# Kernel optimization log

Measured on AMD Instinct MI355X. Metric: run time of the kernel, lower is better.

Reference implementation:

```python
import jax, jax.numpy as jnp
import numpy as np

H = 16
D_MODEL = 1024
B, S = 2, 2048
DH = D_MODEL // H


def setup_inputs() -> dict:
    key = jax.random.key(0)
    ks = jax.random.split(key, 12)
    std = 0.02
    q = jax.random.normal(ks[0], (B, S, D_MODEL), dtype=jnp.float32)
    k = jax.random.normal(ks[1], (B, S, D_MODEL), dtype=jnp.float32)
    v = jax.random.normal(ks[2], (B, S, D_MODEL), dtype=jnp.float32)
    # additive causal mask: 0 on/below diagonal, -1e9 above
    causal = jnp.tril(jnp.ones((S, S), dtype=bool))
    mask = jnp.where(causal, 0.0, -1e9).astype(jnp.float32)[None, None, :, :]
    def dense(kk):
        return (jax.random.normal(kk, (D_MODEL, D_MODEL), dtype=jnp.float32) * std,
                jnp.zeros((D_MODEL,), dtype=jnp.float32))
    Wq, bq = dense(ks[3])
    Wk, bk = dense(ks[4])
    Wv, bv = dense(ks[5])
    Wo, bo = dense(ks[6])
    return {"q": q, "k": k, "v": v, "mask": mask,
            "Wq": Wq, "bq": bq, "Wk": Wk, "bk": bk,
            "Wv": Wv, "bv": bv, "Wo": Wo, "bo": bo}


def reference(q, k, v, mask, Wq, bq, Wk, bk, Wv, bv, Wo, bo):
    b, s, d = q.shape
    def split_heads(x):  # [b,s,d] -> [b,h,s,dh]
        return x.reshape(b, s, H, DH).transpose(0, 2, 1, 3)
    qh = split_heads(q @ Wq + bq)
    kh = split_heads(k @ Wk + bk)
    vh = split_heads(v @ Wv + bv)
    scale = 1.0 / jnp.sqrt(jnp.asarray(DH, dtype=qh.dtype))
    scores = jnp.einsum('bhqd,bhkd->bhqk', qh, kh) * scale + mask
    weights = jax.nn.softmax(scores, axis=-1)
    ctx = jnp.einsum('bhqk,bhkd->bhqd', weights, vh)
    ctx = ctx.transpose(0, 2, 1, 3).reshape(b, s, d)
    return ctx @ Wo + bo
```

## Files before the change

kernel.cpp:

```cpp
#include <hip/hip_runtime.h>
#include <hip/hip_bf16.h>
#include <stdint.h>

typedef __bf16 bf16x8 __attribute__((ext_vector_type(8)));
typedef float  f32x4  __attribute__((ext_vector_type(4)));
typedef __hip_bfloat16 bf16_t;

#define D_MODEL 1024
#define NH 16
#define DH 64
#define BB 2
#define SS 2048
#define MTOT (BB*SS)
#define NQT (SS/64)

#define GBM 128
#define GBN 128
#define GBK 64

__global__ void cvt_qkv_kernel(const float* __restrict__ q, const float* __restrict__ k,
                               const float* __restrict__ v, bf16_t* __restrict__ dst) {
  const int n1v = MTOT * D_MODEL / 4;
  int tid = blockIdx.x * blockDim.x + threadIdx.x;
  int stride = gridDim.x * blockDim.x;
  for (int i = tid; i < 3 * n1v; i += stride) {
    int which = i / n1v;
    int j = i - which * n1v;
    const float4* src = (const float4*)(which == 0 ? q : (which == 1 ? k : v));
    float4 f = src[j];
    union { bf16_t h[4]; short4 s4; } u;
    u.h[0] = __float2bfloat16(f.x);
    u.h[1] = __float2bfloat16(f.y);
    u.h[2] = __float2bfloat16(f.z);
    u.h[3] = __float2bfloat16(f.w);
    ((short4*)dst)[(size_t)which * n1v + j] = u.s4;
  }
}

__global__ void transpose_w_kernel(const float* __restrict__ W0, const float* __restrict__ W1,
                                   const float* __restrict__ W2, const float* __restrict__ W3,
                                   bf16_t* __restrict__ WtAll) {
  __shared__ float tile[32][33];
  const int z = blockIdx.z;
  const float* W = (z == 0) ? W0 : (z == 1) ? W1 : (z == 2) ? W2 : W3;
  bf16_t* Wt = WtAll + (size_t)z * D_MODEL * D_MODEL;
  const int tx = threadIdx.x, ty = threadIdx.y;
  const int bx = blockIdx.x, by = blockIdx.y;
#pragma unroll
  for (int i = 0; i < 4; ++i)
    tile[ty + i * 8][tx] = W[(size_t)(by * 32 + ty + i * 8) * D_MODEL + bx * 32 + tx];
  __syncthreads();
#pragma unroll
  for (int i = 0; i < 4; ++i)
    Wt[(size_t)(bx * 32 + ty + i * 8) * D_MODEL + by * 32 + tx] =
        __float2bfloat16(tile[tx][ty + i * 8]);
}

__device__ __forceinline__ void g2lds16(const bf16_t* g, bf16_t* l) {
  __builtin_amdgcn_global_load_lds((__attribute__((address_space(1))) void*)(g),
                                   (__attribute__((address_space(3))) void*)(l), 16, 0, 0);
}

__device__ __forceinline__ void gemm_tile_mainloop(const bf16_t* __restrict__ A,
                                                   const bf16_t* __restrict__ Bt,
                                                   bf16_t* As, bf16_t* Bs,
                                                   int m0, int n0, f32x4 acc[4][4]) {
  const int tid = threadIdx.x;
  const int wv = tid >> 6, ln = tid & 63;
  const int wr = wv >> 1, wc = wv & 1;
  const int lr = ln & 15, lg = ln >> 4;

#pragma unroll
  for (int mi = 0; mi < 4; ++mi)
#pragma unroll
    for (int ni = 0; ni < 4; ++ni)
      acc[mi][ni] = (f32x4){0.f, 0.f, 0.f, 0.f};

  for (int kt = 0; kt < D_MODEL / GBK; ++kt) {
#pragma unroll
    for (int c = 0; c < 4; ++c) {
      int chunk = wv * 4 + c;
      int row = chunk * 8 + (ln >> 3);
      int col = (ln & 7) * 8;
      g2lds16(A  + (size_t)(m0 + row) * D_MODEL + kt * GBK + col, As + chunk * 8 * GBK);
      g2lds16(Bt + (size_t)(n0 + row) * D_MODEL + kt * GBK + col, Bs + chunk * 8 * GBK);
    }
    __syncthreads();
#pragma unroll
    for (int ks = 0; ks < 2; ++ks) {
      bf16x8 af[4], bfr[4];
#pragma unroll
      for (int mi = 0; mi < 4; ++mi)
        af[mi] = *(const bf16x8*)(As + (size_t)(wr * 64 + mi * 16 + lr) * GBK + ks * 32 + lg * 8);
#pragma unroll
      for (int ni = 0; ni < 4; ++ni)
        bfr[ni] = *(const bf16x8*)(Bs + (size_t)(wc * 64 + ni * 16 + lr) * GBK + ks * 32 + lg * 8);
#pragma unroll
      for (int mi = 0; mi < 4; ++mi)
#pragma unroll
        for (int ni = 0; ni < 4; ++ni)
          acc[mi][ni] = __builtin_amdgcn_mfma_f32_16x16x32_bf16(af[mi], bfr[ni], acc[mi][ni], 0, 0, 0);
    }
    __syncthreads();
  }
}

__global__ __launch_bounds__(256)
void proj_gemm_kernel(const bf16_t* __restrict__ Aq, const bf16_t* __restrict__ Ak,
                      const bf16_t* __restrict__ Av, const bf16_t* __restrict__ WtAll,
                      const float* __restrict__ bq, const float* __restrict__ bk,
                      const float* __restrict__ bv,
                      bf16_t* __restrict__ Qg, bf16_t* __restrict__ Kg,
                      bf16_t* __restrict__ Vt) {
  __shared__ bf16_t As[GBM * GBK];
  __shared__ bf16_t Bs[GBN * GBK];
  const int z = blockIdx.z;
  const bf16_t* A = (z == 0) ? Aq : (z == 1) ? Ak : Av;
  const bf16_t* Bt = WtAll + (size_t)z * D_MODEL * D_MODEL;
  const float* bias = (z == 0) ? bq : (z == 1) ? bk : bv;
  const int m0 = blockIdx.y * GBM, n0 = blockIdx.x * GBN;

  f32x4 acc[4][4];
  gemm_tile_mainloop(A, Bt, As, Bs, m0, n0, acc);

  const int tid = threadIdx.x;
  const int wv = tid >> 6, ln = tid & 63;
  const int wr = wv >> 1, wc = wv & 1;
  const int lr = ln & 15, lg = ln >> 4;

#pragma unroll
  for (int mi = 0; mi < 4; ++mi) {
#pragma unroll
    for (int ni = 0; ni < 4; ++ni) {
      int ncol = n0 + wc * 64 + ni * 16 + lr;
      float bsv = bias[ncol];
#pragma unroll
      for (int j = 0; j < 4; ++j) {
        int mrow = m0 + wr * 64 + mi * 16 + lg * 4 + j;
        bf16_t hv = __float2bfloat16(acc[mi][ni][j] + bsv);
        if (z == 0) {
          Qg[(size_t)mrow * D_MODEL + ncol] = hv;
        } else if (z == 1) {
          Kg[(size_t)mrow * D_MODEL + ncol] = hv;
        } else {
          int b = mrow >> 11, s = mrow & (SS - 1);
          Vt[(size_t)((b << 10) | ncol) * SS + s] = hv;
        }
      }
    }
  }
}

__global__ __launch_bounds__(256)
void out_gemm_kernel(const bf16_t* __restrict__ Ctx, const bf16_t* __restrict__ Wto,
                     const float* __restrict__ bo, float* __restrict__ out) {
  __shared__ bf16_t As[GBM * GBK];
  __shared__ bf16_t Bs[GBN * GBK];
  const int m0 = blockIdx.y * GBM, n0 = blockIdx.x * GBN;

  f32x4 acc[4][4];
  gemm_tile_mainloop(Ctx, Wto, As, Bs, m0, n0, acc);

  const int tid = threadIdx.x;
  const int wv = tid >> 6, ln = tid & 63;
  const int wr = wv >> 1, wc = wv & 1;
  const int lr = ln & 15, lg = ln >> 4;

#pragma unroll
  for (int mi = 0; mi < 4; ++mi) {
#pragma unroll
    for (int ni = 0; ni < 4; ++ni) {
      int ncol = n0 + wc * 64 + ni * 16 + lr;
      float bsv = bo[ncol];
#pragma unroll
      for (int j = 0; j < 4; ++j) {
        int mrow = m0 + wr * 64 + mi * 16 + lg * 4 + j;
        out[(size_t)mrow * D_MODEL + ncol] = acc[mi][ni][j] + bsv;
      }
    }
  }
}

__global__ __launch_bounds__(128)
void attn_kernel(const bf16_t* __restrict__ Qg, const bf16_t* __restrict__ Kg,
                 const bf16_t* __restrict__ Vt, bf16_t* __restrict__ Ctx) {
  __shared__ __align__(16) bf16_t P_lds[2][32][72];
  const int bh = blockIdx.x;
  const int pr = blockIdx.y;
  const int b = bh >> 4, h = bh & 15;
  const int wv = threadIdx.x >> 6, ln = threadIdx.x & 63;
  const int lr = ln & 15, lg = ln >> 4;

  const size_t qkbase = (size_t)b * SS * D_MODEL + (size_t)h * DH;
  const bf16_t* Kbase = Kg + qkbase;
  const bf16_t* Vbase = Vt + (size_t)(bh * 64) * SS;

  bf16x8 onesf;
#pragma unroll
  for (int j = 0; j < 8; ++j) onesf[j] = (__bf16)1.0f;

  for (int half = 0; half < 2; ++half) {
    const int qt = half ? (NQT - 1 - pr) : pr;
    const int q0 = qt * 64 + wv * 32;

    bf16x8 qf[2][2];
#pragma unroll
    for (int mi = 0; mi < 2; ++mi)
#pragma unroll
      for (int ks = 0; ks < 2; ++ks) {
        bf16x8 raw = *(const bf16x8*)(Qg + qkbase + (size_t)(q0 + mi * 16 + lr) * D_MODEL + ks * 32 + lg * 8);
#pragma unroll
        for (int j = 0; j < 8; ++j) raw[j] = (__bf16)((float)raw[j] * 0.125f);
        qf[mi][ks] = raw;
      }

    f32x4 acc_o[2][4];
    f32x4 acc_l[2];
    float m_run[2][4];
#pragma unroll
    for (int mi = 0; mi < 2; ++mi) {
#pragma unroll
      for (int db = 0; db < 4; ++db) acc_o[mi][db] = (f32x4){0.f, 0.f, 0.f, 0.f};
      acc_l[mi] = (f32x4){0.f, 0.f, 0.f, 0.f};
#pragma unroll
      for (int j = 0; j < 4; ++j) m_run[mi][j] = -1e30f;
    }

    bf16x8 kf_cur[2][4];
#pragma unroll
    for (int ks = 0; ks < 2; ++ks)
#pragma unroll
      for (int kb = 0; kb < 4; ++kb)
        kf_cur[ks][kb] = *(const bf16x8*)(Kbase + (size_t)(kb * 16 + lr) * D_MODEL + ks * 32 + lg * 8);

    const int ntiles = qt + 1;
    for (int t = 0; t < ntiles; ++t) {
      const int kv0 = t * 64;
      f32x4 sc[2][4];
#pragma unroll
      for (int mi = 0; mi < 2; ++mi)
#pragma unroll
        for (int kb = 0; kb < 4; ++kb) sc[mi][kb] = (f32x4){0.f, 0.f, 0.f, 0.f};

      __builtin_amdgcn_s_setprio(1);
#pragma unroll
      for (int ks = 0; ks < 2; ++ks) {
#pragma unroll
        for (int kb = 0; kb < 4; ++kb) {
          sc[0][kb] = __builtin_amdgcn_mfma_f32_16x16x32_bf16(qf[0][ks], kf_cur[ks][kb], sc[0][kb], 0, 0, 0);
          sc[1][kb] = __builtin_amdgcn_mfma_f32_16x16x32_bf16(qf[1][ks], kf_cur[ks][kb], sc[1][kb], 0, 0, 0);
        }
      }
      __builtin_amdgcn_s_setprio(0);

      bf16x8 kf_nxt[2][4];
      if (t + 1 < ntiles) {
#pragma unroll
        for (int ks = 0; ks < 2; ++ks)
#pragma unroll
          for (int kb = 0; kb < 4; ++kb)
            kf_nxt[ks][kb] = *(const bf16x8*)(Kbase + (size_t)(kv0 + 64 + kb * 16 + lr) * D_MODEL + ks * 32 + lg * 8);
      }
      bf16x8 vf[2][4];
#pragma unroll
      for (int ks = 0; ks < 2; ++ks)
#pragma unroll
        for (int db = 0; db < 4; ++db)
          vf[ks][db] = *(const bf16x8*)(Vbase + (size_t)(db * 16 + lr) * SS + kv0 + ks * 32 + lg * 8);

      if (kv0 + 63 > q0) {
#pragma unroll
        for (int mi = 0; mi < 2; ++mi)
#pragma unroll
          for (int kb = 0; kb < 4; ++kb)
#pragma unroll
            for (int j = 0; j < 4; ++j) {
              int kc = kv0 + kb * 16 + lr;
              int qr = q0 + mi * 16 + lg * 4 + j;
              if (kc > qr) sc[mi][kb][j] = -1e30f;
            }
      }

#pragma unroll
      for (int mi = 0; mi < 2; ++mi) {
#pragma unroll
        for (int j = 0; j < 4; ++j) {
          float vmax = fmaxf(fmaxf(sc[mi][0][j], sc[mi][1][j]), fmaxf(sc[mi][2][j], sc[mi][3][j]));
#pragma unroll
          for (int off = 1; off < 16; off <<= 1) vmax = fmaxf(vmax, __shfl_xor(vmax, off, 64));
          float mo = m_run[mi][j];
          float mn = fmaxf(mo, vmax);
          float scl = __expf(mo - mn);
          m_run[mi][j] = mn;
#pragma unroll
          for (int kb = 0; kb < 4; ++kb) {
            float p = __expf(sc[mi][kb][j] - mn);
            P_lds[wv][mi * 16 + lg * 4 + j][kb * 16 + lr] = __float2bfloat16(p);
          }
          acc_l[mi][j] *= scl;
#pragma unroll
          for (int db = 0; db < 4; ++db) acc_o[mi][db][j] *= scl;
        }
      }

      asm volatile("s_waitcnt lgkmcnt(0)" ::: "memory");
      __builtin_amdgcn_sched_barrier(0);

      __builtin_amdgcn_s_setprio(1);
#pragma unroll
      for (int ks = 0; ks < 2; ++ks) {
        bf16x8 pa0 = *(const bf16x8*)(&P_lds[wv][lr][ks * 32 + lg * 8]);
        bf16x8 pa1 = *(const bf16x8*)(&P_lds[wv][16 + lr][ks * 32 + lg * 8]);
        acc_l[0] = __builtin_amdgcn_mfma_f32_16x16x32_bf16(pa0, onesf, acc_l[0], 0, 0, 0);
        acc_l[1] = __builtin_amdgcn_mfma_f32_16x16x32_bf16(pa1, onesf, acc_l[1], 0, 0, 0);
#pragma unroll
        for (int db = 0; db < 4; ++db) {
          acc_o[0][db] = __builtin_amdgcn_mfma_f32_16x16x32_bf16(pa0, vf[ks][db], acc_o[0][db], 0, 0, 0);
          acc_o[1][db] = __builtin_amdgcn_mfma_f32_16x16x32_bf16(pa1, vf[ks][db], acc_o[1][db], 0, 0, 0);
        }
      }
      __builtin_amdgcn_s_setprio(0);

      if (t + 1 < ntiles) {
#pragma unroll
        for (int ks = 0; ks < 2; ++ks)
#pragma unroll
          for (int kb = 0; kb < 4; ++kb)
            kf_cur[ks][kb] = kf_nxt[ks][kb];
      }
    }

#pragma unroll
    for (int mi = 0; mi < 2; ++mi)
#pragma unroll
      for (int db = 0; db < 4; ++db)
#pragma unroll
        for (int j = 0; j < 4; ++j) {
          int qr = q0 + mi * 16 + lg * 4 + j;
          float val = acc_o[mi][db][j] / acc_l[mi][j];
          Ctx[(size_t)(b * SS + qr) * D_MODEL + h * DH + db * 16 + lr] = __float2bfloat16(val);
        }
  }
}

extern "C" void kernel_launch(void* const* d_in, const int* in_sizes, int n_in,
                              void* d_out, int out_size, void* d_ws, size_t ws_size,
                              hipStream_t stream) {
  const float* q  = (const float*)d_in[0];
  const float* k  = (const float*)d_in[1];
  const float* v  = (const float*)d_in[2];
  const float* bq = (const float*)d_in[5];
  const float* bk = (const float*)d_in[7];
  const float* bv = (const float*)d_in[9];
  const float* bo = (const float*)d_in[11];
  const float* Wq = (const float*)d_in[4];
  const float* Wk = (const float*)d_in[6];
  const float* Wv = (const float*)d_in[8];
  const float* Wo = (const float*)d_in[10];
  float* out = (float*)d_out;

  char* w = (char*)d_ws;
  bf16_t* Aqkv  = (bf16_t*)(w);
  bf16_t* WtAll = (bf16_t*)(w + 25165824);
  bf16_t* Qg    = (bf16_t*)(w + 33554432);
  bf16_t* Kg    = (bf16_t*)(w + 41943040);
  bf16_t* Vt    = (bf16_t*)(w + 50331648);
  bf16_t* Ctx   = (bf16_t*)(w + 58720256);

  cvt_qkv_kernel<<<2048, 256, 0, stream>>>(q, k, v, Aqkv);
  transpose_w_kernel<<<dim3(32, 32, 4), dim3(32, 8), 0, stream>>>(Wq, Wk, Wv, Wo, WtAll);
  proj_gemm_kernel<<<dim3(8, 32, 3), 256, 0, stream>>>(
      Aqkv, Aqkv + (size_t)MTOT * D_MODEL, Aqkv + 2 * (size_t)MTOT * D_MODEL,
      WtAll, bq, bk, bv, Qg, Kg, Vt);
  attn_kernel<<<dim3(32, 16), 128, 0, stream>>>(Qg, Kg, Vt, Ctx);
  out_gemm_kernel<<<dim3(8, 32), 256, 0, stream>>>(
      Ctx, WtAll + 3 * (size_t)D_MODEL * D_MODEL, bo, out);
}
```

Measured before the change: 299.1 us.

## Split attention KV range across four waves with split-K softmax merge

The attention block now runs four waves instead of two. Waves 0-1 process the low query tile and then the first part of the high tile's KV range. Waves 2-3 process the remaining KV tiles of the high query tile. Their partial O, max and sum are combined through shared memory with a log-sum-exp merge. The aim is to balance work and double the waves per block so the long causal rows finish sooner, at the cost of extra LDS, a block barrier and the merge arithmetic.

```diff
diff --git a/kernel.cpp b/kernel.cpp
--- a/kernel.cpp
+++ b/kernel.cpp
@@ -181,17 +181,156 @@
   }
 }
 
-__global__ __launch_bounds__(128)
+__device__ __forceinline__ void attn_run(
+    f32x4 acc_o[2][4], f32x4 acc_l[2], float m_run[2][4],
+    const bf16x8 qf[2][2], const bf16_t* Kbase, const bf16_t* Vbase,
+    bf16_t (*P)[72], int q0, int t0, int t1, int lr, int lg, bf16x8 onesf) {
+  bf16x8 kf_cur[2][4];
+#pragma unroll
+  for (int ks = 0; ks < 2; ++ks)
+#pragma unroll
+    for (int kb = 0; kb < 4; ++kb)
+      kf_cur[ks][kb] = *(const bf16x8*)(Kbase + (size_t)(t0 * 64 + kb * 16 + lr) * D_MODEL + ks * 32 + lg * 8);
+
+  for (int t = t0; t < t1; ++t) {
+    const int kv0 = t * 64;
+    f32x4 sc[2][4];
+#pragma unroll
+    for (int mi = 0; mi < 2; ++mi)
+#pragma unroll
+      for (int kb = 0; kb < 4; ++kb) sc[mi][kb] = (f32x4){0.f, 0.f, 0.f, 0.f};
+
+    __builtin_amdgcn_s_setprio(1);
+#pragma unroll
+    for (int ks = 0; ks < 2; ++ks) {
+#pragma unroll
+      for (int kb = 0; kb < 4; ++kb) {
+        sc[0][kb] = __builtin_amdgcn_mfma_f32_16x16x32_bf16(qf[0][ks], kf_cur[ks][kb], sc[0][kb], 0, 0, 0);
+        sc[1][kb] = __builtin_amdgcn_mfma_f32_16x16x32_bf16(qf[1][ks], kf_cur[ks][kb], sc[1][kb], 0, 0, 0);
+      }
+    }
+    __builtin_amdgcn_s_setprio(0);
+
+    bf16x8 kf_nxt[2][4];
+    if (t + 1 < t1) {
+#pragma unroll
+      for (int ks = 0; ks < 2; ++ks)
+#pragma unroll
+        for (int kb = 0; kb < 4; ++kb)
+          kf_nxt[ks][kb] = *(const bf16x8*)(Kbase + (size_t)(kv0 + 64 + kb * 16 + lr) * D_MODEL + ks * 32 + lg * 8);
+    }
+    bf16x8 vf[2][4];
+#pragma unroll
+    for (int ks = 0; ks < 2; ++ks)
+#pragma unroll
+      for (int db = 0; db < 4; ++db)
+        vf[ks][db] = *(const bf16x8*)(Vbase + (size_t)(db * 16 + lr) * SS + kv0 + ks * 32 + lg * 8);
+
+    if (kv0 + 63 > q0) {
+#pragma unroll
+      for (int mi = 0; mi < 2; ++mi)
+#pragma unroll
+        for (int kb = 0; kb < 4; ++kb)
+#pragma unroll
+          for (int j = 0; j < 4; ++j) {
+            int kc = kv0 + kb * 16 + lr;
+            int qr = q0 + mi * 16 + lg * 4 + j;
+            if (kc > qr) sc[mi][kb][j] = -1e30f;
+          }
+    }
+
+#pragma unroll
+    for (int mi = 0; mi < 2; ++mi) {
+#pragma unroll
+      for (int j = 0; j < 4; ++j) {
+        float vmax = fmaxf(fmaxf(sc[mi][0][j], sc[mi][1][j]), fmaxf(sc[mi][2][j], sc[mi][3][j]));
+#pragma unroll
+        for (int off = 1; off < 16; off <<= 1) vmax = fmaxf(vmax, __shfl_xor(vmax, off, 64));
+        float mo = m_run[mi][j];
+        float mn = fmaxf(mo, vmax);
+        float scl = __expf(mo - mn);
+        m_run[mi][j] = mn;
+#pragma unroll
+        for (int kb = 0; kb < 4; ++kb) {
+          float p = __expf(sc[mi][kb][j] - mn);
+          P[mi * 16 + lg * 4 + j][kb * 16 + lr] = __float2bfloat16(p);
+        }
+        acc_l[mi][j] *= scl;
+#pragma unroll
+        for (int db = 0; db < 4; ++db) acc_o[mi][db][j] *= scl;
+      }
+    }
+
+    asm volatile("s_waitcnt lgkmcnt(0)" ::: "memory");
+    __builtin_amdgcn_sched_barrier(0);
+
+    __builtin_amdgcn_s_setprio(1);
+#pragma unroll
+    for (int ks = 0; ks < 2; ++ks) {
+      bf16x8 pa0 = *(const bf16x8*)(&P[lr][ks * 32 + lg * 8]);
+      bf16x8 pa1 = *(const bf16x8*)(&P[16 + lr][ks * 32 + lg * 8]);
+      acc_l[0] = __builtin_amdgcn_mfma_f32_16x16x32_bf16(pa0, onesf, acc_l[0], 0, 0, 0);
+      acc_l[1] = __builtin_amdgcn_mfma_f32_16x16x32_bf16(pa1, onesf, acc_l[1], 0, 0, 0);
+#pragma unroll
+      for (int db = 0; db < 4; ++db) {
+        acc_o[0][db] = __builtin_amdgcn_mfma_f32_16x16x32_bf16(pa0, vf[ks][db], acc_o[0][db], 0, 0, 0);
+        acc_o[1][db] = __builtin_amdgcn_mfma_f32_16x16x32_bf16(pa1, vf[ks][db], acc_o[1][db], 0, 0, 0);
+      }
+    }
+    __builtin_amdgcn_s_setprio(0);
+
+    if (t + 1 < t1) {
+#pragma unroll
+      for (int ks = 0; ks < 2; ++ks)
+#pragma unroll
+        for (int kb = 0; kb < 4; ++kb)
+          kf_cur[ks][kb] = kf_nxt[ks][kb];
+    }
+  }
+}
+
+__device__ __forceinline__ void attn_load_q(bf16x8 qf[2][2], const bf16_t* Qbase,
+                                            int q0, int lr, int lg) {
+#pragma unroll
+  for (int mi = 0; mi < 2; ++mi)
+#pragma unroll
+    for (int ks = 0; ks < 2; ++ks) {
+      bf16x8 raw = *(const bf16x8*)(Qbase + (size_t)(q0 + mi * 16 + lr) * D_MODEL + ks * 32 + lg * 8);
+#pragma unroll
+      for (int j = 0; j < 8; ++j) raw[j] = (__bf16)((float)raw[j] * 0.125f);
+      qf[mi][ks] = raw;
+    }
+}
+
+__device__ __forceinline__ void attn_init(f32x4 acc_o[2][4], f32x4 acc_l[2], float m_run[2][4]) {
+#pragma unroll
+  for (int mi = 0; mi < 2; ++mi) {
+#pragma unroll
+    for (int db = 0; db < 4; ++db) acc_o[mi][db] = (f32x4){0.f, 0.f, 0.f, 0.f};
+    acc_l[mi] = (f32x4){0.f, 0.f, 0.f, 0.f};
+#pragma unroll
+    for (int j = 0; j < 4; ++j) m_run[mi][j] = -1e30f;
+  }
+}
+
+__global__ __launch_bounds__(256)
 void attn_kernel(const bf16_t* __restrict__ Qg, const bf16_t* __restrict__ Kg,
                  const bf16_t* __restrict__ Vt, bf16_t* __restrict__ Ctx) {
-  __shared__ __align__(16) bf16_t P_lds[2][32][72];
+  __shared__ __align__(16) bf16_t P_lds[4][32][72];
+  __shared__ __align__(16) float  O_part[2][32][68];
+  __shared__ float  ml_part[2][32][2];
   const int bh = blockIdx.x;
-  const int pr = blockIdx.y;
+  const int pp = blockIdx.y;
   const int b = bh >> 4, h = bh & 15;
   const int wv = threadIdx.x >> 6, ln = threadIdx.x & 63;
   const int lr = ln & 15, lg = ln >> 4;
 
+  const int qt_lo = pp, qt_hi = NQT - 1 - pp;
+  const int h0 = 16 - pp;
+  const int rh = wv & 1;
+
   const size_t qkbase = (size_t)b * SS * D_MODEL + (size_t)h * DH;
+  const bf16_t* Qbase = Qg + qkbase;
   const bf16_t* Kbase = Kg + qkbase;
   const bf16_t* Vbase = Vt + (size_t)(bh * 64) * SS;
 
@@ -199,147 +338,72 @@
 #pragma unroll
   for (int j = 0; j < 8; ++j) onesf[j] = (__bf16)1.0f;
 
-  for (int half = 0; half < 2; ++half) {
-    const int qt = half ? (NQT - 1 - pr) : pr;
-    const int q0 = qt * 64 + wv * 32;
-
-    bf16x8 qf[2][2];
+  bf16x8 qf[2][2];
+  f32x4 acc_o[2][4];
+  f32x4 acc_l[2];
+  float m_run[2][4];
+  const int q0_hi = qt_hi * 64 + rh * 32;
+
+  if (wv < 2) {
+    const int q0_lo = qt_lo * 64 + rh * 32;
+    attn_load_q(qf, Qbase, q0_lo, lr, lg);
+    attn_init(acc_o, acc_l, m_run);
+    attn_run(acc_o, acc_l, m_run, qf, Kbase, Vbase, P_lds[wv], q0_lo, 0, pp + 1, lr, lg, onesf);
 #pragma unroll
     for (int mi = 0; mi < 2; ++mi)
 #pragma unroll
-      for (int ks = 0; ks < 2; ++ks) {
-        bf16x8 raw = *(const bf16x8*)(Qg + qkbase + (size_t)(q0 + mi * 16 + lr) * D_MODEL + ks * 32 + lg * 8);
-#pragma unroll
-        for (int j = 0; j < 8; ++j) raw[j] = (__bf16)((float)raw[j] * 0.125f);
-        qf[mi][ks] = raw;
-      }
-
-    f32x4 acc_o[2][4];
-    f32x4 acc_l[2];
-    float m_run[2][4];
-#pragma unroll
-    for (int mi = 0; mi < 2; ++mi) {
-#pragma unroll
-      for (int db = 0; db < 4; ++db) acc_o[mi][db] = (f32x4){0.f, 0.f, 0.f, 0.f};
-      acc_l[mi] = (f32x4){0.f, 0.f, 0.f, 0.f};
-#pragma unroll
-      for (int j = 0; j < 4; ++j) m_run[mi][j] = -1e30f;
-    }
-
-    bf16x8 kf_cur[2][4];
-#pragma unroll
-    for (int ks = 0; ks < 2; ++ks)
-#pragma unroll
-      for (int kb = 0; kb < 4; ++kb)
-        kf_cur[ks][kb] = *(const bf16x8*)(Kbase + (size_t)(kb * 16 + lr) * D_MODEL + ks * 32 + lg * 8);
-
-    const int ntiles = qt + 1;
-    for (int t = 0; t < ntiles; ++t) {
-      const int kv0 = t * 64;
-      f32x4 sc[2][4];
-#pragma unroll
-      for (int mi = 0; mi < 2; ++mi)
-#pragma unroll
-        for (int kb = 0; kb < 4; ++kb) sc[mi][kb] = (f32x4){0.f, 0.f, 0.f, 0.f};
-
-      __builtin_amdgcn_s_setprio(1);
-#pragma unroll
-      for (int ks = 0; ks < 2; ++ks) {
-#pragma unroll
-        for (int kb = 0; kb < 4; ++kb) {
-          sc[0][kb] = __builtin_amdgcn_mfma_f32_16x16x32_bf16(qf[0][ks], kf_cur[ks][kb], sc[0][kb], 0, 0, 0);
-          sc[1][kb] = __builtin_amdgcn_mfma_f32_16x16x32_bf16(qf[1][ks], kf_cur[ks][kb], sc[1][kb], 0, 0, 0);
-        }
-      }
-      __builtin_amdgcn_s_setprio(0);
-
-      bf16x8 kf_nxt[2][4];
-      if (t + 1 < ntiles) {
-#pragma unroll
-        for (int ks = 0; ks < 2; ++ks)
-#pragma unroll
-          for (int kb = 0; kb < 4; ++kb)
-            kf_nxt[ks][kb] = *(const bf16x8*)(Kbase + (size_t)(kv0 + 64 + kb * 16 + lr) * D_MODEL + ks * 32 + lg * 8);
-      }
-      bf16x8 vf[2][4];
-#pragma unroll
-      for (int ks = 0; ks < 2; ++ks)
-#pragma unroll
-        for (int db = 0; db < 4; ++db)
-          vf[ks][db] = *(const bf16x8*)(Vbase + (size_t)(db * 16 + lr) * SS + kv0 + ks * 32 + lg * 8);
-
-      if (kv0 + 63 > q0) {
-#pragma unroll
-        for (int mi = 0; mi < 2; ++mi)
-#pragma unroll
-          for (int kb = 0; kb < 4; ++kb)
-#pragma unroll
-            for (int j = 0; j < 4; ++j) {
-              int kc = kv0 + kb * 16 + lr;
-              int qr = q0 + mi * 16 + lg * 4 + j;
-              if (kc > qr) sc[mi][kb][j] = -1e30f;
-            }
-      }
-
-#pragma unroll
-      for (int mi = 0; mi < 2; ++mi) {
+      for (int db = 0; db < 4; ++db)
 #pragma unroll
         for (int j = 0; j < 4; ++j) {
-          float vmax = fmaxf(fmaxf(sc[mi][0][j], sc[mi][1][j]), fmaxf(sc[mi][2][j], sc[mi][3][j]));
-#pragma unroll
-          for (int off = 1; off < 16; off <<= 1) vmax = fmaxf(vmax, __shfl_xor(vmax, off, 64));
-          float mo = m_run[mi][j];
-          float mn = fmaxf(mo, vmax);
-          float scl = __expf(mo - mn);
-          m_run[mi][j] = mn;
-#pragma unroll
-          for (int kb = 0; kb < 4; ++kb) {
-            float p = __expf(sc[mi][kb][j] - mn);
-            P_lds[wv][mi * 16 + lg * 4 + j][kb * 16 + lr] = __float2bfloat16(p);
-          }
-          acc_l[mi][j] *= scl;
-#pragma unroll
-          for (int db = 0; db < 4; ++db) acc_o[mi][db][j] *= scl;
-        }
-      }
-
-      asm volatile("s_waitcnt lgkmcnt(0)" ::: "memory");
-      __builtin_amdgcn_sched_barrier(0);
-
-      __builtin_amdgcn_s_setprio(1);
-#pragma unroll
-      for (int ks = 0; ks < 2; ++ks) {
-        bf16x8 pa0 = *(const bf16x8*)(&P_lds[wv][lr][ks * 32 + lg * 8]);
-        bf16x8 pa1 = *(const bf16x8*)(&P_lds[wv][16 + lr][ks * 32 + lg * 8]);
-        acc_l[0] = __builtin_amdgcn_mfma_f32_16x16x32_bf16(pa0, onesf, acc_l[0], 0, 0, 0);
-        acc_l[1] = __builtin_amdgcn_mfma_f32_16x16x32_bf16(pa1, onesf, acc_l[1], 0, 0, 0);
-#pragma unroll
-        for (int db = 0; db < 4; ++db) {
-          acc_o[0][db] = __builtin_amdgcn_mfma_f32_16x16x32_bf16(pa0, vf[ks][db], acc_o[0][db], 0, 0, 0);
-          acc_o[1][db] = __builtin_amdgcn_mfma_f32_16x16x32_bf16(pa1, vf[ks][db], acc_o[1][db], 0, 0, 0);
-        }
-      }
-      __builtin_amdgcn_s_setprio(0);
-
-      if (t + 1 < ntiles) {
-#pragma unroll
-        for (int ks = 0; ks < 2; ++ks)
-#pragma unroll
-          for (int kb = 0; kb < 4; ++kb)
-            kf_cur[ks][kb] = kf_nxt[ks][kb];
-      }
-    }
-
-#pragma unroll
-    for (int mi = 0; mi < 2; ++mi)
-#pragma unroll
-      for (int db = 0; db < 4; ++db)
-#pragma unroll
-        for (int j = 0; j < 4; ++j) {
-          int qr = q0 + mi * 16 + lg * 4 + j;
+          int qr = q0_lo + mi * 16 + lg * 4 + j;
           float val = acc_o[mi][db][j] / acc_l[mi][j];
           Ctx[(size_t)(b * SS + qr) * D_MODEL + h * DH + db * 16 + lr] = __float2bfloat16(val);
         }
+
+    attn_load_q(qf, Qbase, q0_hi, lr, lg);
+    attn_init(acc_o, acc_l, m_run);
+    attn_run(acc_o, acc_l, m_run, qf, Kbase, Vbase, P_lds[wv], q0_hi, 0, h0, lr, lg, onesf);
+  } else {
+    attn_load_q(qf, Qbase, q0_hi, lr, lg);
+    attn_init(acc_o, acc_l, m_run);
+    attn_run(acc_o, acc_l, m_run, qf, Kbase, Vbase, P_lds[wv], q0_hi, h0, NQT - pp, lr, lg, onesf);
+    const int pidx = wv - 2;
+#pragma unroll
+    for (int mi = 0; mi < 2; ++mi)
+#pragma unroll
+      for (int j = 0; j < 4; ++j) {
+        int r = mi * 16 + lg * 4 + j;
+#pragma unroll
+        for (int db = 0; db < 4; ++db)
+          O_part[pidx][r][db * 16 + lr] = acc_o[mi][db][j];
+        if (lr == 0) {
+          ml_part[pidx][r][0] = m_run[mi][j];
+          ml_part[pidx][r][1] = acc_l[mi][j];
+        }
+      }
+  }
+
+  __syncthreads();
+
+  if (wv < 2) {
+#pragma unroll
+    for (int mi = 0; mi < 2; ++mi)
+#pragma unroll
+      for (int j = 0; j < 4; ++j) {
+        int r = mi * 16 + lg * 4 + j;
+        float m1 = m_run[mi][j];
+        float m2 = ml_part[wv][r][0];
+        float mn = fmaxf(m1, m2);
+        float a1 = __expf(m1 - mn);
+        float a2 = __expf(m2 - mn);
+        float l = a1 * acc_l[mi][j] + a2 * ml_part[wv][r][1];
+        int qr = q0_hi + r;
+#pragma unroll
+        for (int db = 0; db < 4; ++db) {
+          float val = (a1 * acc_o[mi][db][j] + a2 * O_part[wv][r][db * 16 + lr]) / l;
+          Ctx[(size_t)(b * SS + qr) * D_MODEL + h * DH + db * 16 + lr] = __float2bfloat16(val);
+        }
+      }
   }
 }
 
@@ -372,7 +436,7 @@
   proj_gemm_kernel<<<dim3(8, 32, 3), 256, 0, stream>>>(
       Aqkv, Aqkv + (size_t)MTOT * D_MODEL, Aqkv + 2 * (size_t)MTOT * D_MODEL,
       WtAll, bq, bk, bv, Qg, Kg, Vt);
-  attn_kernel<<<dim3(32, 16), 128, 0, stream>>>(Qg, Kg, Vt, Ctx);
+  attn_kernel<<<dim3(32, 16), 256, 0, stream>>>(Qg, Kg, Vt, Ctx);
   out_gemm_kernel<<<dim3(8, 32), 256, 0, stream>>>(
       Ctx, WtAll + 3 * (size_t)D_MODEL * D_MODEL, bo, out);
 }
```

After: 295.1 us. Within noise of the previous version (-1.3%).
